# Performance work log

Hardware: AMD Instinct MI355X
Metric: run time of the kernel (lower is better)

## Reference

```python
import jax, jax.numpy as jnp
import numpy as np

WS = 8          # window size
SHIFT = WS // 2 # cyclic shift for shifted windows
HEADS = 6
C = 192
EMB = 256
HID = 4 * C
EPS = 1e-5


def _inorm(x):
    # InstanceNorm2d (affine=False): normalize each (sample, channel) over spatial dims
    m = x.mean(axis=(2, 3), keepdims=True)
    v = x.var(axis=(2, 3), keepdims=True)
    return (x - m) * jax.lax.rsqrt(v + EPS)


def _rel_index(ws):
    c = jnp.stack(jnp.meshgrid(jnp.arange(ws), jnp.arange(ws), indexing='ij'), -1).reshape(-1, 2)
    r = c[:, None] - c[None, :] + (ws - 1)          # (N,N,2) in [0, 2ws-2]
    return r[..., 0] * (2 * ws - 1) + r[..., 1]     # (N,N)


def _attn_mask(H, W, ws, shift):
    # standard Swin shifted-window mask: tokens from different pre-shift regions can't attend
    def ids(L):
        a = jnp.arange(L)
        return (a >= L - ws).astype(jnp.int32) + (a >= L - shift).astype(jnp.int32)
    img = ids(H)[:, None] * 3 + ids(W)[None, :]                     # (H,W)
    imgw = img.reshape(H // ws, ws, W // ws, ws).transpose(0, 2, 1, 3).reshape(-1, ws * ws)  # (nW,N)
    return jnp.where(imgw[:, None, :] != imgw[:, :, None], -1e9, 0.0)  # (nW,N,N)


def setup_inputs() -> dict:
    key = jax.random.key(0)
    ks = jax.random.split(key, 12)
    s = 0.02
    return {
        'x':        jax.random.normal(ks[0], (8, C, 128, 128), jnp.float32),
        'cond':     jax.random.normal(ks[1], (8, EMB), jnp.float32),
        'qkv_w':    jax.random.normal(ks[2], (3 * C, C), jnp.float32) * s,
        'qkv_b':    jnp.zeros((3 * C,), jnp.float32),
        'proj_w':   jax.random.normal(ks[3], (C, C), jnp.float32) * s,
        'proj_b':   jnp.zeros((C,), jnp.float32),
        'rel_bias': jax.random.normal(ks[4], ((2 * WS - 1) ** 2, HEADS), jnp.float32) * s,
        'film_w':   jax.random.normal(ks[5], (2 * C, EMB), jnp.float32) * s,
        'film_b':   jnp.zeros((2 * C,), jnp.float32),
        'mlp_w1':   jax.random.normal(ks[6], (HID, C), jnp.float32) * s,
        'mlp_b1':   jnp.zeros((HID,), jnp.float32),
        'mlp_w2':   jax.random.normal(ks[7], (C, HID), jnp.float32) * s,
        'mlp_b2':   jnp.zeros((C,), jnp.float32),
    }


def reference(x, cond, qkv_w, qkv_b, proj_w, proj_b, rel_bias,
              film_w, film_b, mlp_w1, mlp_b1, mlp_w2, mlp_b2):
    B, Cc, H, W = x.shape
    N = WS * WS
    nW = (H // WS) * (W // WS)
    hd = Cc // HEADS

    # ---- x = x + attn(norm1(x)) : shifted window attention ----
    xn = _inorm(x)
    xs = jnp.roll(xn, (-SHIFT, -SHIFT), axis=(2, 3))
    # window partition -> (B, nW, N, C)
    xw = (xs.reshape(B, Cc, H // WS, WS, W // WS, WS)
            .transpose(0, 2, 4, 3, 5, 1)
            .reshape(B, nW, N, Cc))
    qkv = xw @ qkv_w.T + qkv_b                       # (B,nW,N,3C)
    q, k, v = jnp.split(qkv, 3, axis=-1)
    def heads(t):
        return t.reshape(B, nW, N, HEADS, hd).transpose(0, 1, 3, 2, 4)  # (B,nW,H,N,hd)
    q, k, v = heads(q), heads(k), heads(v)
    attn = jnp.einsum('bwhnd,bwhmd->bwhnm', q, k) * (hd ** -0.5)
    bias = rel_bias[_rel_index(WS)].transpose(2, 0, 1)   # (HEADS,N,N)
    mask = _attn_mask(H, W, WS, SHIFT)                   # (nW,N,N)
    attn = attn + bias[None, None] + mask[None, :, None]
    a = jax.nn.softmax(attn, axis=-1)
    o = jnp.einsum('bwhnm,bwhmd->bwhnd', a, v)
    o = o.transpose(0, 1, 3, 2, 4).reshape(B, nW, N, Cc)
    o = o @ proj_w.T + proj_b
    # window reverse -> (B,C,H,W), undo shift
    o = (o.reshape(B, H // WS, W // WS, WS, WS, Cc)
           .transpose(0, 5, 1, 3, 2, 4)
           .reshape(B, Cc, H, W))
    o = jnp.roll(o, (SHIFT, SHIFT), axis=(2, 3))
    x = x + o

    # ---- x = x + mlp(FiLM(norm2(x), cond)) ----
    h = _inorm(x)
    gb = cond @ film_w.T + film_b                     # (B,2C)
    scale, shift = gb[:, :Cc], gb[:, Cc:]
    h = h * (1.0 + scale)[:, :, None, None] + shift[:, :, None, None]
    h = jnp.einsum('bchw,oc->bohw', h, mlp_w1) + mlp_b1[None, :, None, None]
    h = jax.nn.gelu(h, approximate=True)              # GELU('tanh')
    h = jnp.einsum('bchw,oc->bohw', h, mlp_w2) + mlp_b2[None, :, None, None]
    return x + h
```

## Files before the change

kernel.cpp:

```cpp
#include <hip/hip_runtime.h>
#include <hip/hip_bf16.h>

using bf16 = __hip_bfloat16;

#define HEADS 6
#define EPSV 1e-5f
#define QS 0.17677669529663687f

typedef __bf16 bfv8 __attribute__((ext_vector_type(8)));
typedef short sv8 __attribute__((ext_vector_type(8)));
typedef float fv4 __attribute__((ext_vector_type(4)));

__device__ __forceinline__ unsigned short f2bfbits(float f) {
  union { float f; unsigned u; } x{f};
  unsigned r = x.u + 0x7fffu + ((x.u >> 16) & 1u);
  return (unsigned short)(r >> 16);
}

__device__ __forceinline__ int swz(int row, int col, int rowstride) {
  return row * rowstride + ((((col >> 3) ^ (row & 7)) << 3) | (col & 7));
}

__device__ __forceinline__ uint2 pack4b(fv4 a, float b0, float b1, float b2, float b3) {
  uint2 r;
  r.x = (unsigned)f2bfbits(a[0] + b0) | ((unsigned)f2bfbits(a[1] + b1) << 16);
  r.y = (unsigned)f2bfbits(a[2] + b2) | ((unsigned)f2bfbits(a[3] + b3) << 16);
  return r;
}

template <bool BW>
__device__ __forceinline__ bfv8 ldwf(const short* wb, const float* wf, int row,
                                     int k, int ld, float scale) {
  if constexpr (BW) {
    return *(const bfv8*)(wb + (size_t)row * ld + k);
  } else {
    const float* p = wf + (size_t)row * ld + k;
    float4 a = *(const float4*)p;
    float4 b = *(const float4*)(p + 4);
    sv8 s;
    s[0] = (short)f2bfbits(a.x * scale); s[1] = (short)f2bfbits(a.y * scale);
    s[2] = (short)f2bfbits(a.z * scale); s[3] = (short)f2bfbits(a.w * scale);
    s[4] = (short)f2bfbits(b.x * scale); s[5] = (short)f2bfbits(b.y * scale);
    s[6] = (short)f2bfbits(b.z * scale); s[7] = (short)f2bfbits(b.w * scale);
    return __builtin_bit_cast(bfv8, s);
  }
}

__device__ __forceinline__ void stats_body(const float* __restrict__ x, int bc,
                                           float2* __restrict__ mr, int tid) {
  const float4* p = (const float4*)(x + (size_t)bc * 16384);
  float s = 0.f, s2 = 0.f;
  for (int i = tid; i < 4096; i += 256) {
    float4 v = p[i];
    s += v.x + v.y + v.z + v.w;
    s2 = fmaf(v.x, v.x, s2);
    s2 = fmaf(v.y, v.y, s2);
    s2 = fmaf(v.z, v.z, s2);
    s2 = fmaf(v.w, v.w, s2);
  }
#pragma unroll
  for (int off = 32; off > 0; off >>= 1) {
    s += __shfl_down(s, off);
    s2 += __shfl_down(s2, off);
  }
  __shared__ float rs[4], rs2[4];
  int wid = tid >> 6;
  if ((tid & 63) == 0) { rs[wid] = s; rs2[wid] = s2; }
  __syncthreads();
  if (tid == 0) {
    float S = rs[0] + rs[1] + rs[2] + rs[3];
    float S2 = rs2[0] + rs2[1] + rs2[2] + rs2[3];
    float m = S * (1.f / 16384.f);
    float v = S2 * (1.f / 16384.f) - m * m;
    mr[bc] = make_float2(m, rsqrtf(v + EPSV));
  }
}

__global__ __launch_bounds__(256) void stats_kernel(const float* __restrict__ x,
                                                    float2* __restrict__ mr) {
  stats_body(x, blockIdx.x, mr, threadIdx.x);
}

__device__ __forceinline__ void pack8(float4 a, float4 b, float sc, short* dst) {
  uint4 o;
  o.x = (unsigned)f2bfbits(a.x * sc) | ((unsigned)f2bfbits(a.y * sc) << 16);
  o.y = (unsigned)f2bfbits(a.z * sc) | ((unsigned)f2bfbits(a.w * sc) << 16);
  o.z = (unsigned)f2bfbits(b.x * sc) | ((unsigned)f2bfbits(b.y * sc) << 16);
  o.w = (unsigned)f2bfbits(b.z * sc) | ((unsigned)f2bfbits(b.w * sc) << 16);
  *(uint4*)dst = o;
}

__global__ __launch_bounds__(256) void fused_pre_kernel(
    const float* __restrict__ x, float2* __restrict__ mr1,
    const float* __restrict__ cond, const float* __restrict__ fw,
    const float* __restrict__ fb, float* __restrict__ gb,
    const float* __restrict__ qkv_w, const float* __restrict__ proj_w,
    const float* __restrict__ mlp_w1, const float* __restrict__ mlp_w2,
    short* __restrict__ wbA, int nUnits) {
  int bid = blockIdx.x;
  if (bid < 1536) {
    stats_body(x, bid, mr1, threadIdx.x);
    return;
  }
  bid -= 1536;
  if (bid < 12) {
    int g = bid * 256 + threadIdx.x;
    if (g >= 8 * 384) return;
    int b = g / 384, o = g % 384;
    const float* c = cond + b * 256;
    const float* w = fw + o * 256;
    float acc = fb[o];
    for (int k = 0; k < 256; k += 4) {
      float4 cv = *(const float4*)(c + k);
      float4 wv = *(const float4*)(w + k);
      acc = fmaf(cv.x, wv.x, acc);
      acc = fmaf(cv.y, wv.y, acc);
      acc = fmaf(cv.z, wv.z, acc);
      acc = fmaf(cv.w, wv.w, acc);
    }
    gb[g] = acc;
    return;
  }
  int u = (bid - 12) * 256 + threadIdx.x;
  if (u >= nUnits) return;
  if (u < 18432) {
    int e = u * 8;
    float sc = (e < 36864) ? QS : 1.f;
    const float* src = (e < 110592) ? (qkv_w + e) : (proj_w + (e - 110592));
    pack8(*(const float4*)src, *(const float4*)(src + 4), sc, wbA + e);
  } else if (u < 36864) {
    int f = (u - 18432) * 8;
    int ob = f / 12288, s = f % 12288;
    int row = s / 192, within = s % 192;
    int col0 = (((within >> 3) ^ (row & 7)) << 3);
    const float* src = mlp_w1 + (size_t)(ob * 64 + row) * 192 + col0;
    pack8(*(const float4*)src, *(const float4*)(src + 4), 1.f, wbA + 147456 + f);
  } else {
    int f = (u - 36864) * 8;
    int ob = f / 12288, s = f % 12288;
    int row = s / 64, within = s % 64;
    int ol = (((within >> 3) ^ (row & 7)) << 3);
    const float* src = mlp_w2 + (size_t)row * 768 + ob * 64 + ol;
    pack8(*(const float4*)src, *(const float4*)(src + 4), 1.f, wbA + 294912 + f);
  }
}

__global__ __launch_bounds__(64) void reduce2_kernel(const float2* __restrict__ part,
                                                     float2* __restrict__ mr2) {
  int bc = blockIdx.x;
  int b = bc / 192, c = bc % 192;
  const float2* p = part + (size_t)(b * 256) * 192 + c;
  float s = 0.f, q = 0.f;
  for (int k = threadIdx.x; k < 256; k += 64) {
    float2 v = p[(size_t)k * 192];
    s += v.x;
    q += v.y;
  }
#pragma unroll
  for (int off = 32; off > 0; off >>= 1) {
    s += __shfl_down(s, off);
    q += __shfl_down(q, off);
  }
  if (threadIdx.x == 0) {
    float m = s * (1.f / 16384.f);
    float v = q * (1.f / 16384.f) - m * m;
    mr2[bc] = make_float2(m, rsqrtf(v + EPSV));
  }
}

template <bool BW>
__global__ __launch_bounds__(512, 2) void attn_mfma4_kernel(
    const float* __restrict__ x, const float2* __restrict__ mr1,
    const short* __restrict__ wb, const float* __restrict__ qkv_w,
    const float* __restrict__ qkv_b, const float* __restrict__ proj_w,
    const float* __restrict__ proj_b, const float* __restrict__ rel_bias,
    float* __restrict__ out, float2* __restrict__ part) {
  __shared__ __align__(16) short s_x[64 * 192];
  __shared__ __align__(16) short s_k[64 * 192];
  __shared__ __align__(16) short s_v[192 * 64];
  __shared__ float s_rel[1350];

  const short* wbq = wb;
  const short* wbp = wb + 110592;

  int tid = threadIdx.x;
  int blk = ((blockIdx.x & 7) << 8) + (blockIdx.x >> 3);
  int b = blk >> 8;
  int wdw = blk & 255;
  int wh = wdw >> 4, ww = wdw & 15;
  int lane = tid & 63;
  int w = tid >> 6;
  int nloc = lane & 15, lg = lane >> 4;

  for (int i = tid; i < 1350; i += 512) s_rel[i] = rel_bias[i];

  for (int u = tid; u < 3072; u += 512) {
    int jh = u & 1, ii = (u >> 1) & 7, c = u >> 4;
    int hg = (wh * 8 + ii + 4) & 127;
    int wc0 = (ww * 8 + jh * 4 + 4) & 127;
    float4 v = *(const float4*)&x[((size_t)(b * 192 + c) << 14) + (hg << 7) + wc0];
    float2 mrv = mr1[b * 192 + c];
    int n0 = ii * 8 + jh * 4;
    s_x[swz(n0 + 0, c, 192)] = (short)f2bfbits((v.x - mrv.x) * mrv.y);
    s_x[swz(n0 + 1, c, 192)] = (short)f2bfbits((v.y - mrv.x) * mrv.y);
    s_x[swz(n0 + 2, c, 192)] = (short)f2bfbits((v.z - mrv.x) * mrv.y);
    s_x[swz(n0 + 3, c, 192)] = (short)f2bfbits((v.w - mrv.x) * mrv.y);
  }
  __syncthreads();

  for (int half = 0; half < 2; half++) {
    int ptb = half * 2;
    bfv8 xf[2][6];
#pragma unroll
    for (int pp = 0; pp < 2; pp++)
#pragma unroll
      for (int ks = 0; ks < 6; ks++)
        xf[pp][ks] = *(const bfv8*)&s_x[swz((ptb + pp) * 16 + nloc, ks * 32 + lg * 8, 192)];
    __syncthreads();

    bfv8 wf[6];
    {
      int t0 = w;
      int baserow0 = (t0 < 24) ? t0 * 16 : 384 + (t0 - 24) * 16;
      float scl0 = (!BW && t0 < 12) ? QS : 1.f;
#pragma unroll
      for (int ks = 0; ks < 6; ks++)
        wf[ks] = ldwf<BW>(wbq, qkv_w, baserow0 + nloc, ks * 32 + lg * 8, 192, scl0);
    }
    for (int t = w; t < 36;) {
      int tn = t + 8;
      bfv8 wfn[6];
      if (tn < 36) {
        int baserown = (tn < 24) ? tn * 16 : 384 + (tn - 24) * 16;
        float scln = (!BW && tn < 12) ? QS : 1.f;
#pragma unroll
        for (int ks = 0; ks < 6; ks++)
          wfn[ks] = ldwf<BW>(wbq, qkv_w, baserown + nloc, ks * 32 + lg * 8, 192, scln);
      }
      bool isQK = (t < 24);
#pragma unroll
      for (int pp = 0; pp < 2; pp++) {
        int pt = ptb + pp;
        fv4 acc = fv4{0.f, 0.f, 0.f, 0.f};
        if (isQK) {
#pragma unroll
          for (int ks = 0; ks < 6; ks++)
            acc = __builtin_amdgcn_mfma_f32_16x16x32_bf16(wf[ks], xf[pp][ks], acc, 0, 0, 0);
          int o0 = t * 16 + lg * 4;
          float4 bb = *(const float4*)&qkv_b[o0];
          float bsc = (t < 12) ? QS : 1.f;
          uint2 pkk = pack4b(acc, bb.x * bsc, bb.y * bsc, bb.z * bsc, bb.w * bsc);
          if (t < 12)
            *(uint2*)&s_x[swz(pt * 16 + nloc, o0, 192)] = pkk;
          else
            *(uint2*)&s_k[swz(pt * 16 + nloc, o0 - 192, 192)] = pkk;
        } else {
#pragma unroll
          for (int ks = 0; ks < 6; ks++)
            acc = __builtin_amdgcn_mfma_f32_16x16x32_bf16(xf[pp][ks], wf[ks], acc, 0, 0, 0);
          int d = (t - 24) * 16 + nloc;
          float bv = qkv_b[384 + d];
          *(uint2*)&s_v[swz(d, pt * 16 + lg * 4, 64)] = pack4b(acc, bv, bv, bv, bv);
        }
      }
      if (tn >= 36) break;
#pragma unroll
      for (int ks = 0; ks < 6; ks++) wf[ks] = wfn[ks];
      t = tn;
    }
  }
  __syncthreads();

  int maskh = (wh == 15), maskw = (ww == 15);
#pragma unroll
  for (int ui = 0; ui < 3; ui++) {
    int u = w * 3 + ui;
    int hh = u >> 2, ng = u & 3;
    int n = ng * 16 + nloc;
    int i1 = n >> 3, j1 = n & 7;
    int gn = (maskh ? (i1 < 4 ? 1 : 2) : 0) * 3 + (maskw ? (j1 < 4 ? 1 : 2) : 0);

    bfv8 qf = *(const bfv8*)&s_x[swz(n, hh * 32 + lg * 8, 192)];
    fv4 sc[4];
#pragma unroll
    for (int mt = 0; mt < 4; mt++) {
      bfv8 kf = *(const bfv8*)&s_k[swz(mt * 16 + nloc, hh * 32 + lg * 8, 192)];
      sc[mt] = __builtin_amdgcn_mfma_f32_16x16x32_bf16(kf, qf, fv4{0.f, 0.f, 0.f, 0.f}, 0, 0, 0);
    }
    bfv8 vfh[2][2];
#pragma unroll
    for (int dt = 0; dt < 2; dt++)
#pragma unroll
      for (int ks = 0; ks < 2; ks++)
        vfh[dt][ks] = *(const bfv8*)&s_v[swz(hh * 32 + dt * 16 + nloc, ks * 32 + lg * 8, 64)];

    float vals[16];
#pragma unroll
    for (int mt = 0; mt < 4; mt++) {
#pragma unroll
      for (int r = 0; r < 4; r++) {
        int m = mt * 16 + lg * 4 + r;
        int i2 = m >> 3, j2 = m & 7;
        int gm = (maskh ? (i2 < 4 ? 1 : 2) : 0) * 3 + (maskw ? (j2 < 4 ? 1 : 2) : 0);
        float v = sc[mt][r] + s_rel[((i1 - i2 + 7) * 15 + (j1 - j2 + 7)) * 6 + hh];
        vals[mt * 4 + r] = (gn == gm) ? v : v - 1e9f;
      }
    }
    float mx = vals[0];
#pragma unroll
    for (int q = 1; q < 16; q++) mx = fmaxf(mx, vals[q]);
    mx = fmaxf(mx, __shfl_xor(mx, 16));
    mx = fmaxf(mx, __shfl_xor(mx, 32));
    float sum = 0.f;
#pragma unroll
    for (int q = 0; q < 16; q++) {
      vals[q] = __expf(vals[q] - mx);
      sum += vals[q];
    }
    sum += __shfl_xor(sum, 16);
    sum += __shfl_xor(sum, 32);
    float inv = 1.f / sum;

    unsigned pk[4][2];
#pragma unroll
    for (int mt = 0; mt < 4; mt++) {
      pk[mt][0] = (unsigned)f2bfbits(vals[mt * 4] * inv) |
                  ((unsigned)f2bfbits(vals[mt * 4 + 1] * inv) << 16);
      pk[mt][1] = (unsigned)f2bfbits(vals[mt * 4 + 2] * inv) |
                  ((unsigned)f2bfbits(vals[mt * 4 + 3] * inv) << 16);
    }
    int sel = lg >> 1;
    int S0 = nloc + ((lg & 1) << 5);
    int S1 = S0 + 16;
    bfv8 pf[2];
#pragma unroll
    for (int ks = 0; ks < 2; ks++) {
      unsigned a0 = (unsigned)__shfl((int)pk[2 * ks][0], S0);
      unsigned b0 = (unsigned)__shfl((int)pk[2 * ks + 1][0], S0);
      unsigned a1 = (unsigned)__shfl((int)pk[2 * ks][1], S0);
      unsigned b1 = (unsigned)__shfl((int)pk[2 * ks + 1][1], S0);
      unsigned a2 = (unsigned)__shfl((int)pk[2 * ks][0], S1);
      unsigned b2 = (unsigned)__shfl((int)pk[2 * ks + 1][0], S1);
      unsigned a3 = (unsigned)__shfl((int)pk[2 * ks][1], S1);
      unsigned b3 = (unsigned)__shfl((int)pk[2 * ks + 1][1], S1);
      uint4 uu;
      uu.x = sel ? b0 : a0;
      uu.y = sel ? b1 : a1;
      uu.z = sel ? b2 : a2;
      uu.w = sel ? b3 : a3;
      pf[ks] = __builtin_bit_cast(bfv8, uu);
    }
#pragma unroll
    for (int dt = 0; dt < 2; dt++) {
      fv4 oa = fv4{0.f, 0.f, 0.f, 0.f};
#pragma unroll
      for (int ks = 0; ks < 2; ks++)
        oa = __builtin_amdgcn_mfma_f32_16x16x32_bf16(vfh[dt][ks], pf[ks], oa, 0, 0, 0);
      int d0 = hh * 32 + dt * 16 + lg * 4;
      *(uint2*)&s_x[swz(n, d0, 192)] = pack4b(oa, 0.f, 0.f, 0.f, 0.f);
    }
  }
  __syncthreads();

  {
    int a2 = w >> 1, half = w & 1;
    int hgv[2], wcv[2];
#pragma unroll
    for (int ni = 0; ni < 2; ni++) {
      int n = (half * 2 + ni) * 16 + nloc;
      hgv[ni] = (wh * 8 + (n >> 3) + 4) & 127;
      wcv[ni] = (ww * 8 + (n & 7) + 4) & 127;
    }
    float* redS = (float*)s_rel;
    float* redQ = redS + 384;

#pragma unroll
    for (int ci = 0; ci < 3; ci++) {
      int ct = a2 * 3 + ci;
      bfv8 wfp[6];
#pragma unroll
      for (int ks = 0; ks < 6; ks++)
        wfp[ks] = ldwf<BW>(wbp, proj_w, ct * 16 + nloc, ks * 32 + lg * 8, 192, 1.f);
      float xres[2][4];
#pragma unroll
      for (int ni = 0; ni < 2; ni++)
#pragma unroll
        for (int r = 0; r < 4; r++) {
          int c = ct * 16 + lg * 4 + r;
          xres[ni][r] = x[((size_t)(b * 192 + c) << 14) + (hgv[ni] << 7) + wcv[ni]];
        }
      float4 pb4 = *(const float4*)&proj_b[ct * 16 + lg * 4];
      const float* pbp = &pb4.x;
      float ssum[4] = {0.f, 0.f, 0.f, 0.f};
      float ssq[4] = {0.f, 0.f, 0.f, 0.f};
#pragma unroll
      for (int ni = 0; ni < 2; ni++) {
        int nt = half * 2 + ni;
        fv4 acc = fv4{0.f, 0.f, 0.f, 0.f};
#pragma unroll
        for (int ks = 0; ks < 6; ks++) {
          bfv8 of = *(const bfv8*)&s_x[swz(nt * 16 + nloc, ks * 32 + lg * 8, 192)];
          acc = __builtin_amdgcn_mfma_f32_16x16x32_bf16(wfp[ks], of, acc, 0, 0, 0);
        }
#pragma unroll
        for (int r = 0; r < 4; r++) {
          int c = ct * 16 + lg * 4 + r;
          size_t gi = ((size_t)(b * 192 + c) << 14) + (hgv[ni] << 7) + wcv[ni];
          float v = xres[ni][r] + acc[r] + pbp[r];
          out[gi] = v;
          ssum[r] += v;
          ssq[r] = fmaf(v, v, ssq[r]);
        }
      }
      if (part) {
#pragma unroll
        for (int r = 0; r < 4; r++) {
          float s = ssum[r], q = ssq[r];
#pragma unroll
          for (int m = 1; m < 16; m <<= 1) {
            s += __shfl_xor(s, m);
            q += __shfl_xor(q, m);
          }
          if (nloc == 0) {
            int c = ct * 16 + lg * 4 + r;
            redS[c * 2 + half] = s;
            redQ[c * 2 + half] = q;
          }
        }
      }
    }

    if (part) {
      __syncthreads();
      if (tid < 192) {
        float s = redS[tid * 2] + redS[tid * 2 + 1];
        float q = redQ[tid * 2] + redQ[tid * 2 + 1];
        part[(size_t)blk * 192 + tid] = make_float2(s, q);
      }
    }
  }
}

__global__ __launch_bounds__(512, 2) void mlp_mfma3_kernel(
    float* __restrict__ xio, const float2* __restrict__ mr2,
    const float* __restrict__ gb, const short* __restrict__ w1s,
    const short* __restrict__ w2s, const float* __restrict__ b1,
    const float* __restrict__ b2) {
  __shared__ __align__(16) short s_pool[128 * 192];
  __shared__ __align__(16) short s_h[128 * 64];
  __shared__ float s_b1[768];
  __shared__ float s_mean[192], s_rstd[192], s_scale[192], s_shift[192], s_b2[192];

  int tid = threadIdx.x;
  int blk = blockIdx.x;
  int b = blk >> 7;
  int p0 = (blk & 127) << 7;
  int lane = tid & 63;
  int w = tid >> 6;

  for (int i = tid; i < 768; i += 512) s_b1[i] = b1[i];
  for (int i = tid; i < 192; i += 512) {
    float2 mrv = mr2[b * 192 + i];
    s_mean[i] = mrv.x;
    s_rstd[i] = mrv.y;
    s_scale[i] = 1.f + gb[b * 384 + i];
    s_shift[i] = gb[b * 384 + 192 + i];
    s_b2[i] = b2[i];
  }
  __syncthreads();

  for (int e = tid; e < 768; e += 512) {
    int pq = e & 31, cb = e >> 5;
    int p = pq * 4, c0 = cb * 8;
    float4 xv[8];
#pragma unroll
    for (int j = 0; j < 8; j++)
      xv[j] = *(const float4*)&xio[((size_t)(b * 192 + c0 + j) << 14) + p0 + p];
#pragma unroll
    for (int j = 0; j < 8; j++) {
      int c = c0 + j;
      float mn = s_mean[c], rs = s_rstd[c], scv = s_scale[c], sh = s_shift[c];
      xv[j].x = (xv[j].x - mn) * rs * scv + sh;
      xv[j].y = (xv[j].y - mn) * rs * scv + sh;
      xv[j].z = (xv[j].z - mn) * rs * scv + sh;
      xv[j].w = (xv[j].w - mn) * rs * scv + sh;
    }
#pragma unroll
    for (int pp = 0; pp < 4; pp++) {
      sv8 pk;
#pragma unroll
      for (int j = 0; j < 8; j++) pk[j] = (short)f2bfbits((&xv[j].x)[pp]);
      *(sv8*)&s_pool[swz(p + pp, c0, 192)] = pk;
    }
  }
  __syncthreads();

  int prow = w * 16 + (lane & 15);
  bfv8 afr[6];
#pragma unroll
  for (int ks = 0; ks < 6; ks++) {
    int c = ks * 32 + (lane >> 4) * 8;
    afr[ks] = *(const bfv8*)&s_pool[swz(prow, c, 192)];
  }

  short* s_w1 = s_pool;
  short* s_w2 = s_pool + 12288;
  char* poolBytes = (char*)s_pool;

  fv4 acc2[12];
#pragma unroll
  for (int i = 0; i < 12; i++) acc2[i] = fv4{0.f, 0.f, 0.f, 0.f};

  for (int ob = 0; ob < 12; ob++) {
    __syncthreads();
    const char* g1 = (const char*)(w1s + ob * 12288);
    const char* g2 = (const char*)(w2s + ob * 12288);
#pragma unroll
    for (int i = 0; i < 3; i++) {
      int ch = w * 3 + i;
      __builtin_amdgcn_global_load_lds(
          (const __attribute__((address_space(1))) void*)(g1 + ch * 1024 + lane * 16),
          (__attribute__((address_space(3))) void*)(poolBytes + ch * 1024), 16, 0, 0);
      __builtin_amdgcn_global_load_lds(
          (const __attribute__((address_space(1))) void*)(g2 + ch * 1024 + lane * 16),
          (__attribute__((address_space(3))) void*)(poolBytes + 24576 + ch * 1024), 16, 0, 0);
    }
    __syncthreads();

#pragma unroll
    for (int it = 0; it < 4; it++) {
      fv4 a1 = fv4{0.f, 0.f, 0.f, 0.f};
      int orow = it * 16 + (lane & 15);
#pragma unroll
      for (int ks = 0; ks < 6; ks++) {
        int c = ks * 32 + (lane >> 4) * 8;
        bfv8 wf = *(const bfv8*)&s_w1[swz(orow, c, 192)];
        a1 = __builtin_amdgcn_mfma_f32_16x16x32_bf16(wf, afr[ks], a1, 0, 0, 0);
      }
      int o0 = ob * 64 + it * 16 + (lane >> 4) * 4;
      unsigned short hb[4];
#pragma unroll
      for (int r = 0; r < 4; r++) {
        float v = a1[r] + s_b1[o0 + r];
        float g = v / (1.f + __expf(-1.5957691216f * fmaf(0.044715f * v * v, v, v)));
        hb[r] = f2bfbits(g);
      }
      uint2 pk;
      pk.x = (unsigned)hb[0] | ((unsigned)hb[1] << 16);
      pk.y = (unsigned)hb[2] | ((unsigned)hb[3] << 16);
      int ol = it * 16 + (lane >> 4) * 4;
      *(uint2*)&s_h[swz(prow, ol, 64)] = pk;
    }

#pragma unroll
    for (int ks2 = 0; ks2 < 2; ks2++) {
      int ol = ks2 * 32 + (lane >> 4) * 8;
      bfv8 hf = *(const bfv8*)&s_h[swz(prow, ol, 64)];
#pragma unroll
      for (int it2 = 0; it2 < 12; it2++) {
        int crow = it2 * 16 + (lane & 15);
        bfv8 w2f = *(const bfv8*)&s_w2[swz(crow, ol, 64)];
        acc2[it2] = __builtin_amdgcn_mfma_f32_16x16x32_bf16(w2f, hf, acc2[it2], 0, 0, 0);
      }
    }
  }

  int p = p0 + w * 16 + (lane & 15);
#pragma unroll
  for (int it2 = 0; it2 < 12; it2++) {
    int c0 = it2 * 16 + (lane >> 4) * 4;
#pragma unroll
    for (int r = 0; r < 4; r++) {
      int c = c0 + r;
      size_t gi = ((size_t)(b * 192 + c) << 14) + p;
      xio[gi] += acc2[it2][r] + s_b2[c];
    }
  }
}

__global__ __launch_bounds__(512, 2) void mlp_mfma_kernel(
    float* __restrict__ xio, const float2* __restrict__ mr2,
    const float* __restrict__ gb, const float* __restrict__ w1,
    const float* __restrict__ b1, const float* __restrict__ w2,
    const float* __restrict__ b2) {
  __shared__ __align__(16) short s_a[128 * 192];
  __shared__ __align__(16) short s_h[128 * 64];
  __shared__ __align__(16) short s_w1[64 * 192];
  __shared__ __align__(16) short s_w2[192 * 64];
  __shared__ float s_b1[768];
  __shared__ float s_mean[192], s_rstd[192], s_scale[192], s_shift[192], s_b2[192];

  int tid = threadIdx.x;
  int blk = blockIdx.x;
  int b = blk >> 7;
  int p0 = (blk & 127) << 7;
  int lane = tid & 63;
  int w = tid >> 6;

  for (int i = tid; i < 768; i += 512) s_b1[i] = b1[i];
  for (int i = tid; i < 192; i += 512) {
    float2 mrv = mr2[b * 192 + i];
    s_mean[i] = mrv.x;
    s_rstd[i] = mrv.y;
    s_scale[i] = 1.f + gb[b * 384 + i];
    s_shift[i] = gb[b * 384 + 192 + i];
    s_b2[i] = b2[i];
  }
  __syncthreads();

  for (int e = tid; e < 3072; e += 512) {
    int p = e & 127, cb = e >> 7;
    int c0 = cb * 8;
    sv8 pk;
#pragma unroll
    for (int j = 0; j < 8; j++) {
      int c = c0 + j;
      float xv = xio[((size_t)(b * 192 + c) << 14) + p0 + p];
      float hn = (xv - s_mean[c]) * s_rstd[c];
      pk[j] = (short)f2bfbits(hn * s_scale[c] + s_shift[c]);
    }
    *(sv8*)&s_a[swz(p, c0, 192)] = pk;
  }
  __syncthreads();

  int prow = w * 16 + (lane & 15);
  bfv8 afr[6];
#pragma unroll
  for (int ks = 0; ks < 6; ks++) {
    int c = ks * 32 + (lane >> 4) * 8;
    afr[ks] = *(const bfv8*)&s_a[swz(prow, c, 192)];
  }

  fv4 acc2[12];
#pragma unroll
  for (int i = 0; i < 12; i++) acc2[i] = fv4{0.f, 0.f, 0.f, 0.f};

  for (int ob = 0; ob < 12; ob++) {
    __syncthreads();
    for (int e = tid; e < 3072; e += 512) {
      int row = e / 48, ch4 = e % 48;
      float4 v = *(const float4*)&w1[(size_t)(ob * 64 + row) * 192 + ch4 * 4];
      uint2 pk;
      pk.x = (unsigned)f2bfbits(v.x) | ((unsigned)f2bfbits(v.y) << 16);
      pk.y = (unsigned)f2bfbits(v.z) | ((unsigned)f2bfbits(v.w) << 16);
      *(uint2*)&s_w1[swz(row, ch4 * 4, 192)] = pk;
    }
    for (int e = tid; e < 3072; e += 512) {
      int row = e >> 4, o4 = (e & 15) * 4;
      float4 v = *(const float4*)&w2[(size_t)row * 768 + ob * 64 + o4];
      uint2 pk;
      pk.x = (unsigned)f2bfbits(v.x) | ((unsigned)f2bfbits(v.y) << 16);
      pk.y = (unsigned)f2bfbits(v.z) | ((unsigned)f2bfbits(v.w) << 16);
      *(uint2*)&s_w2[swz(row, o4, 64)] = pk;
    }
    __syncthreads();

#pragma unroll
    for (int it = 0; it < 4; it++) {
      fv4 a1 = fv4{0.f, 0.f, 0.f, 0.f};
      int orow = it * 16 + (lane & 15);
#pragma unroll
      for (int ks = 0; ks < 6; ks++) {
        int c = ks * 32 + (lane >> 4) * 8;
        bfv8 wf = *(const bfv8*)&s_w1[swz(orow, c, 192)];
        a1 = __builtin_amdgcn_mfma_f32_16x16x32_bf16(wf, afr[ks], a1, 0, 0, 0);
      }
      int o0 = ob * 64 + it * 16 + (lane >> 4) * 4;
      unsigned short hb[4];
#pragma unroll
      for (int r = 0; r < 4; r++) {
        float v = a1[r] + s_b1[o0 + r];
        float g = v / (1.f + __expf(-1.5957691216f * fmaf(0.044715f * v * v, v, v)));
        hb[r] = f2bfbits(g);
      }
      uint2 pk;
      pk.x = (unsigned)hb[0] | ((unsigned)hb[1] << 16);
      pk.y = (unsigned)hb[2] | ((unsigned)hb[3] << 16);
      int ol = it * 16 + (lane >> 4) * 4;
      *(uint2*)&s_h[swz(prow, ol, 64)] = pk;
    }

#pragma unroll
    for (int ks2 = 0; ks2 < 2; ks2++) {
      int ol = ks2 * 32 + (lane >> 4) * 8;
      bfv8 hf = *(const bfv8*)&s_h[swz(prow, ol, 64)];
#pragma unroll
      for (int it2 = 0; it2 < 12; it2++) {
        int crow = it2 * 16 + (lane & 15);
        bfv8 w2f = *(const bfv8*)&s_w2[swz(crow, ol, 64)];
        acc2[it2] = __builtin_amdgcn_mfma_f32_16x16x32_bf16(w2f, hf, acc2[it2], 0, 0, 0);
      }
    }
  }

  int p = p0 + w * 16 + (lane & 15);
#pragma unroll
  for (int it2 = 0; it2 < 12; it2++) {
    int c0 = it2 * 16 + (lane >> 4) * 4;
#pragma unroll
    for (int r = 0; r < 4; r++) {
      int c = c0 + r;
      size_t gi = ((size_t)(b * 192 + c) << 14) + p;
      xio[gi] += acc2[it2][r] + s_b2[c];
    }
  }
}

extern "C" void kernel_launch(void* const* d_in, const int* in_sizes, int n_in,
                              void* d_out, int out_size, void* d_ws, size_t ws_size,
                              hipStream_t stream) {
  const float* x = (const float*)d_in[0];
  const float* cond = (const float*)d_in[1];
  const float* qkv_w = (const float*)d_in[2];
  const float* qkv_b = (const float*)d_in[3];
  const float* proj_w = (const float*)d_in[4];
  const float* proj_b = (const float*)d_in[5];
  const float* rel_bias = (const float*)d_in[6];
  const float* film_w = (const float*)d_in[7];
  const float* film_b = (const float*)d_in[8];
  const float* mlp_w1 = (const float*)d_in[9];
  const float* mlp_b1 = (const float*)d_in[10];
  const float* mlp_w2 = (const float*)d_in[11];
  const float* mlp_b2 = (const float*)d_in[12];

  float* out = (float*)d_out;
  char* wsb = (char*)d_ws;

  float2* mr1 = (float2*)wsb;
  float2* mr2 = (float2*)(wsb + 12288);
  float* gb = (float*)(wsb + 24576);
  const size_t base = 36864;
  const size_t partB = 2048ull * 192 * 8;
  const size_t wbB = 442368ull * 2;

  bool fuseP = ws_size >= base + partB + wbB;
  bool haveM = fuseP || ws_size >= base + wbB;
  bool haveA = ws_size >= base + 294912;

  float2* part = fuseP ? (float2*)(wsb + base) : nullptr;
  short* wbA = (short*)(wsb + base + (fuseP ? partB : 0));

  int nUnits = haveM ? 55296 : (haveA ? 18432 : 0);
  fused_pre_kernel<<<1536 + 12 + (nUnits + 255) / 256, 256, 0, stream>>>(
      x, mr1, cond, film_w, film_b, gb, qkv_w, proj_w, mlp_w1, mlp_w2, wbA, nUnits);

  if (haveA)
    attn_mfma4_kernel<true><<<2048, 512, 0, stream>>>(
        x, mr1, wbA, qkv_w, qkv_b, proj_w, proj_b, rel_bias, out, part);
  else
    attn_mfma4_kernel<false><<<2048, 512, 0, stream>>>(
        x, mr1, wbA, qkv_w, qkv_b, proj_w, proj_b, rel_bias, out, part);

  if (part)
    reduce2_kernel<<<1536, 64, 0, stream>>>(part, mr2);
  else
    stats_kernel<<<1536, 256, 0, stream>>>(out, mr2);

  if (haveM)
    mlp_mfma3_kernel<<<1024, 512, 0, stream>>>(out, mr2, gb, wbA + 147456,
                                               wbA + 294912, mlp_b1, mlp_b2);
  else
    mlp_mfma_kernel<<<1024, 512, 0, stream>>>(out, mr2, gb, mlp_w1, mlp_b1,
                                              mlp_w2, mlp_b2);
}
```

Measured before the change: 423.8 us.

## Double-buffer MLP weight staging, raise attention occupancy, drop fused stats partials

The MLP kernel now streams weights in 32-row halves through two LDS buffers, prefetching the next half with global_load_lds while the current one is computed. The mlp_w2 prepack layout is changed to match a 32-column swizzle. The attention kernel gets a launch bound of 4 blocks per CU: it drops the software prefetch of qkv weights, loads V fragments lazily and reads the residual inline, all to cut register pressure. It also adds s_setprio around the MFMA sections. The fused per-window InstanceNorm partial sums and reduce kernel are removed in favour of a separate stats pass over the output, which adds a full extra read of the activation tensor.

```diff
diff --git a/kernel.cpp b/kernel.cpp
--- a/kernel.cpp
+++ b/kernel.cpp
@@ -19,6 +19,10 @@
 
 __device__ __forceinline__ int swz(int row, int col, int rowstride) {
   return row * rowstride + ((((col >> 3) ^ (row & 7)) << 3) | (col & 7));
+}
+
+__device__ __forceinline__ int swz32(int row, int col) {
+  return row * 32 + ((((col >> 3) ^ ((row >> 1) & 3)) << 3) | (col & 7));
 }
 
 __device__ __forceinline__ uint2 pack4b(fv4 a, float b0, float b1, float b2, float b3) {
@@ -137,44 +141,23 @@
     pack8(*(const float4*)src, *(const float4*)(src + 4), 1.f, wbA + 147456 + f);
   } else {
     int f = (u - 36864) * 8;
-    int ob = f / 12288, s = f % 12288;
-    int row = s / 64, within = s % 64;
-    int ol = (((within >> 3) ^ (row & 7)) << 3);
-    const float* src = mlp_w2 + (size_t)row * 768 + ob * 64 + ol;
+    int chunk = f / 6144, s = f % 6144;
+    int r = s / 32, within = s % 32;
+    int blk = within >> 3;
+    int ob = chunk >> 1, ch = chunk & 1;
+    int srccol = ob * 64 + ch * 32 + ((blk ^ ((r >> 1) & 3)) << 3);
+    const float* src = mlp_w2 + (size_t)r * 768 + srccol;
     pack8(*(const float4*)src, *(const float4*)(src + 4), 1.f, wbA + 294912 + f);
   }
 }
 
-__global__ __launch_bounds__(64) void reduce2_kernel(const float2* __restrict__ part,
-                                                     float2* __restrict__ mr2) {
-  int bc = blockIdx.x;
-  int b = bc / 192, c = bc % 192;
-  const float2* p = part + (size_t)(b * 256) * 192 + c;
-  float s = 0.f, q = 0.f;
-  for (int k = threadIdx.x; k < 256; k += 64) {
-    float2 v = p[(size_t)k * 192];
-    s += v.x;
-    q += v.y;
-  }
-#pragma unroll
-  for (int off = 32; off > 0; off >>= 1) {
-    s += __shfl_down(s, off);
-    q += __shfl_down(q, off);
-  }
-  if (threadIdx.x == 0) {
-    float m = s * (1.f / 16384.f);
-    float v = q * (1.f / 16384.f) - m * m;
-    mr2[bc] = make_float2(m, rsqrtf(v + EPSV));
-  }
-}
-
 template <bool BW>
-__global__ __launch_bounds__(512, 2) void attn_mfma4_kernel(
+__global__ __launch_bounds__(512, 4) void attn_mfma5_kernel(
     const float* __restrict__ x, const float2* __restrict__ mr1,
     const short* __restrict__ wb, const float* __restrict__ qkv_w,
     const float* __restrict__ qkv_b, const float* __restrict__ proj_w,
     const float* __restrict__ proj_b, const float* __restrict__ rel_bias,
-    float* __restrict__ out, float2* __restrict__ part) {
+    float* __restrict__ out) {
   __shared__ __align__(16) short s_x[64 * 192];
   __shared__ __align__(16) short s_k[64 * 192];
   __shared__ __align__(16) short s_v[192 * 64];
@@ -218,26 +201,15 @@
         xf[pp][ks] = *(const bfv8*)&s_x[swz((ptb + pp) * 16 + nloc, ks * 32 + lg * 8, 192)];
     __syncthreads();
 
-    bfv8 wf[6];
-    {
-      int t0 = w;
-      int baserow0 = (t0 < 24) ? t0 * 16 : 384 + (t0 - 24) * 16;
-      float scl0 = (!BW && t0 < 12) ? QS : 1.f;
+    for (int t = w; t < 36; t += 8) {
+      bool isQK = (t < 24);
+      int baserow = isQK ? t * 16 : 384 + (t - 24) * 16;
+      float scl = (!BW && t < 12) ? QS : 1.f;
+      bfv8 wf[6];
 #pragma unroll
       for (int ks = 0; ks < 6; ks++)
-        wf[ks] = ldwf<BW>(wbq, qkv_w, baserow0 + nloc, ks * 32 + lg * 8, 192, scl0);
-    }
-    for (int t = w; t < 36;) {
-      int tn = t + 8;
-      bfv8 wfn[6];
-      if (tn < 36) {
-        int baserown = (tn < 24) ? tn * 16 : 384 + (tn - 24) * 16;
-        float scln = (!BW && tn < 12) ? QS : 1.f;
-#pragma unroll
-        for (int ks = 0; ks < 6; ks++)
-          wfn[ks] = ldwf<BW>(wbq, qkv_w, baserown + nloc, ks * 32 + lg * 8, 192, scln);
-      }
-      bool isQK = (t < 24);
+        wf[ks] = ldwf<BW>(wbq, qkv_w, baserow + nloc, ks * 32 + lg * 8, 192, scl);
+      __builtin_amdgcn_s_setprio(1);
 #pragma unroll
       for (int pp = 0; pp < 2; pp++) {
         int pt = ptb + pp;
@@ -263,10 +235,7 @@
           *(uint2*)&s_v[swz(d, pt * 16 + lg * 4, 64)] = pack4b(acc, bv, bv, bv, bv);
         }
       }
-      if (tn >= 36) break;
-#pragma unroll
-      for (int ks = 0; ks < 6; ks++) wf[ks] = wfn[ks];
-      t = tn;
+      __builtin_amdgcn_s_setprio(0);
     }
   }
   __syncthreads();
@@ -282,18 +251,13 @@
 
     bfv8 qf = *(const bfv8*)&s_x[swz(n, hh * 32 + lg * 8, 192)];
     fv4 sc[4];
+    __builtin_amdgcn_s_setprio(1);
 #pragma unroll
     for (int mt = 0; mt < 4; mt++) {
       bfv8 kf = *(const bfv8*)&s_k[swz(mt * 16 + nloc, hh * 32 + lg * 8, 192)];
       sc[mt] = __builtin_amdgcn_mfma_f32_16x16x32_bf16(kf, qf, fv4{0.f, 0.f, 0.f, 0.f}, 0, 0, 0);
     }
-    bfv8 vfh[2][2];
-#pragma unroll
-    for (int dt = 0; dt < 2; dt++)
-#pragma unroll
-      for (int ks = 0; ks < 2; ks++)
-        vfh[dt][ks] = *(const bfv8*)&s_v[swz(hh * 32 + dt * 16 + nloc, ks * 32 + lg * 8, 64)];
-
+    __builtin_amdgcn_s_setprio(0);
     float vals[16];
 #pragma unroll
     for (int mt = 0; mt < 4; mt++) {
@@ -350,104 +314,66 @@
       uu.w = sel ? b3 : a3;
       pf[ks] = __builtin_bit_cast(bfv8, uu);
     }
+    __builtin_amdgcn_s_setprio(1);
 #pragma unroll
     for (int dt = 0; dt < 2; dt++) {
       fv4 oa = fv4{0.f, 0.f, 0.f, 0.f};
 #pragma unroll
-      for (int ks = 0; ks < 2; ks++)
-        oa = __builtin_amdgcn_mfma_f32_16x16x32_bf16(vfh[dt][ks], pf[ks], oa, 0, 0, 0);
+      for (int ks = 0; ks < 2; ks++) {
+        bfv8 vf = *(const bfv8*)&s_v[swz(hh * 32 + dt * 16 + nloc, ks * 32 + lg * 8, 64)];
+        oa = __builtin_amdgcn_mfma_f32_16x16x32_bf16(vf, pf[ks], oa, 0, 0, 0);
+      }
       int d0 = hh * 32 + dt * 16 + lg * 4;
       *(uint2*)&s_x[swz(n, d0, 192)] = pack4b(oa, 0.f, 0.f, 0.f, 0.f);
     }
+    __builtin_amdgcn_s_setprio(0);
   }
   __syncthreads();
 
   {
     int a2 = w >> 1, half = w & 1;
-    int hgv[2], wcv[2];
-#pragma unroll
-    for (int ni = 0; ni < 2; ni++) {
-      int n = (half * 2 + ni) * 16 + nloc;
-      hgv[ni] = (wh * 8 + (n >> 3) + 4) & 127;
-      wcv[ni] = (ww * 8 + (n & 7) + 4) & 127;
-    }
-    float* redS = (float*)s_rel;
-    float* redQ = redS + 384;
-
 #pragma unroll
     for (int ci = 0; ci < 3; ci++) {
       int ct = a2 * 3 + ci;
-      bfv8 wfp[6];
+      bfv8 wf[6];
 #pragma unroll
       for (int ks = 0; ks < 6; ks++)
-        wfp[ks] = ldwf<BW>(wbp, proj_w, ct * 16 + nloc, ks * 32 + lg * 8, 192, 1.f);
-      float xres[2][4];
-#pragma unroll
-      for (int ni = 0; ni < 2; ni++)
-#pragma unroll
-        for (int r = 0; r < 4; r++) {
-          int c = ct * 16 + lg * 4 + r;
-          xres[ni][r] = x[((size_t)(b * 192 + c) << 14) + (hgv[ni] << 7) + wcv[ni]];
-        }
-      float4 pb4 = *(const float4*)&proj_b[ct * 16 + lg * 4];
-      const float* pbp = &pb4.x;
-      float ssum[4] = {0.f, 0.f, 0.f, 0.f};
-      float ssq[4] = {0.f, 0.f, 0.f, 0.f};
+        wf[ks] = ldwf<BW>(wbp, proj_w, ct * 16 + nloc, ks * 32 + lg * 8, 192, 1.f);
 #pragma unroll
       for (int ni = 0; ni < 2; ni++) {
         int nt = half * 2 + ni;
         fv4 acc = fv4{0.f, 0.f, 0.f, 0.f};
+        __builtin_amdgcn_s_setprio(1);
 #pragma unroll
         for (int ks = 0; ks < 6; ks++) {
           bfv8 of = *(const bfv8*)&s_x[swz(nt * 16 + nloc, ks * 32 + lg * 8, 192)];
-          acc = __builtin_amdgcn_mfma_f32_16x16x32_bf16(wfp[ks], of, acc, 0, 0, 0);
+          acc = __builtin_amdgcn_mfma_f32_16x16x32_bf16(wf[ks], of, acc, 0, 0, 0);
         }
+        __builtin_amdgcn_s_setprio(0);
+        int n = nt * 16 + nloc;
+        int ii = n >> 3, jj = n & 7;
+        int hg = (wh * 8 + ii + 4) & 127;
+        int wc = (ww * 8 + jj + 4) & 127;
+        float4 pb4 = *(const float4*)&proj_b[ct * 16 + lg * 4];
+        const float* pbp = &pb4.x;
 #pragma unroll
         for (int r = 0; r < 4; r++) {
           int c = ct * 16 + lg * 4 + r;
-          size_t gi = ((size_t)(b * 192 + c) << 14) + (hgv[ni] << 7) + wcv[ni];
-          float v = xres[ni][r] + acc[r] + pbp[r];
-          out[gi] = v;
-          ssum[r] += v;
-          ssq[r] = fmaf(v, v, ssq[r]);
+          size_t gi = ((size_t)(b * 192 + c) << 14) + (hg << 7) + wc;
+          out[gi] = x[gi] + acc[r] + pbp[r];
         }
       }
-      if (part) {
-#pragma unroll
-        for (int r = 0; r < 4; r++) {
-          float s = ssum[r], q = ssq[r];
-#pragma unroll
-          for (int m = 1; m < 16; m <<= 1) {
-            s += __shfl_xor(s, m);
-            q += __shfl_xor(q, m);
-          }
-          if (nloc == 0) {
-            int c = ct * 16 + lg * 4 + r;
-            redS[c * 2 + half] = s;
-            redQ[c * 2 + half] = q;
-          }
-        }
-      }
-    }
-
-    if (part) {
-      __syncthreads();
-      if (tid < 192) {
-        float s = redS[tid * 2] + redS[tid * 2 + 1];
-        float q = redQ[tid * 2] + redQ[tid * 2 + 1];
-        part[(size_t)blk * 192 + tid] = make_float2(s, q);
-      }
-    }
-  }
-}
-
-__global__ __launch_bounds__(512, 2) void mlp_mfma3_kernel(
+    }
+  }
+}
+
+__global__ __launch_bounds__(512, 2) void mlp_mfma5_kernel(
     float* __restrict__ xio, const float2* __restrict__ mr2,
     const float* __restrict__ gb, const short* __restrict__ w1s,
     const short* __restrict__ w2s, const float* __restrict__ b1,
     const float* __restrict__ b2) {
-  __shared__ __align__(16) short s_pool[128 * 192];
-  __shared__ __align__(16) short s_h[128 * 64];
+  __shared__ __align__(16) short s_pool[2 * 12288];
+  __shared__ __align__(16) short s_h[128 * 32];
   __shared__ float s_b1[768];
   __shared__ float s_mean[192], s_rstd[192], s_scale[192], s_shift[192], s_b2[192];
 
@@ -502,68 +428,83 @@
     int c = ks * 32 + (lane >> 4) * 8;
     afr[ks] = *(const bfv8*)&s_pool[swz(prow, c, 192)];
   }
-
-  short* s_w1 = s_pool;
-  short* s_w2 = s_pool + 12288;
+  __syncthreads();
+
   char* poolBytes = (char*)s_pool;
+  const char* w1B = (const char*)w1s;
+  const char* w2B = (const char*)w2s;
 
   fv4 acc2[12];
 #pragma unroll
   for (int i = 0; i < 12; i++) acc2[i] = fv4{0.f, 0.f, 0.f, 0.f};
 
-  for (int ob = 0; ob < 12; ob++) {
-    __syncthreads();
-    const char* g1 = (const char*)(w1s + ob * 12288);
-    const char* g2 = (const char*)(w2s + ob * 12288);
-#pragma unroll
-    for (int i = 0; i < 3; i++) {
-      int ch = w * 3 + i;
-      __builtin_amdgcn_global_load_lds(
-          (const __attribute__((address_space(1))) void*)(g1 + ch * 1024 + lane * 16),
-          (__attribute__((address_space(3))) void*)(poolBytes + ch * 1024), 16, 0, 0);
-      __builtin_amdgcn_global_load_lds(
-          (const __attribute__((address_space(1))) void*)(g2 + ch * 1024 + lane * 16),
-          (__attribute__((address_space(3))) void*)(poolBytes + 24576 + ch * 1024), 16, 0, 0);
-    }
-    __syncthreads();
-
-#pragma unroll
-    for (int it = 0; it < 4; it++) {
+#define STAGE_HALF(hb, bufIdx)                                                        \
+  {                                                                                   \
+    char* dstB = poolBytes + (bufIdx)*24576;                                          \
+    _Pragma("unroll") for (int j = 0; j < 3; j++) {                                   \
+      int ch = w * 3 + j;                                                             \
+      const char* srcB = (ch < 12) ? (w1B + (size_t)(hb)*12288 + ch * 1024)           \
+                                   : (w2B + (size_t)(hb)*12288 + (ch - 12) * 1024);   \
+      __builtin_amdgcn_global_load_lds(                                               \
+          (const __attribute__((address_space(1))) void*)(srcB + lane * 16),          \
+          (__attribute__((address_space(3))) void*)(dstB + ch * 1024), 16, 0, 0);     \
+    }                                                                                 \
+  }
+
+  STAGE_HALF(0, 0);
+  asm volatile("s_waitcnt vmcnt(0)" ::: "memory");
+  __builtin_amdgcn_s_barrier();
+
+  for (int i = 0; i < 24; ++i) {
+    int cur = i & 1;
+    if (i < 23) STAGE_HALF(i + 1, cur ^ 1);
+
+    const short* bw1 = s_pool + cur * 12288;
+    const short* bw2 = s_pool + cur * 12288 + 6144;
+
+#pragma unroll
+    for (int it = 0; it < 2; it++) {
       fv4 a1 = fv4{0.f, 0.f, 0.f, 0.f};
       int orow = it * 16 + (lane & 15);
+      __builtin_amdgcn_s_setprio(1);
 #pragma unroll
       for (int ks = 0; ks < 6; ks++) {
         int c = ks * 32 + (lane >> 4) * 8;
-        bfv8 wf = *(const bfv8*)&s_w1[swz(orow, c, 192)];
+        bfv8 wf = *(const bfv8*)&bw1[swz(orow, c, 192)];
         a1 = __builtin_amdgcn_mfma_f32_16x16x32_bf16(wf, afr[ks], a1, 0, 0, 0);
       }
-      int o0 = ob * 64 + it * 16 + (lane >> 4) * 4;
-      unsigned short hb[4];
+      __builtin_amdgcn_s_setprio(0);
+      int o0 = i * 32 + it * 16 + (lane >> 4) * 4;
+      unsigned short hbv[4];
 #pragma unroll
       for (int r = 0; r < 4; r++) {
         float v = a1[r] + s_b1[o0 + r];
         float g = v / (1.f + __expf(-1.5957691216f * fmaf(0.044715f * v * v, v, v)));
-        hb[r] = f2bfbits(g);
+        hbv[r] = f2bfbits(g);
       }
       uint2 pk;
-      pk.x = (unsigned)hb[0] | ((unsigned)hb[1] << 16);
-      pk.y = (unsigned)hb[2] | ((unsigned)hb[3] << 16);
+      pk.x = (unsigned)hbv[0] | ((unsigned)hbv[1] << 16);
+      pk.y = (unsigned)hbv[2] | ((unsigned)hbv[3] << 16);
       int ol = it * 16 + (lane >> 4) * 4;
-      *(uint2*)&s_h[swz(prow, ol, 64)] = pk;
-    }
-
-#pragma unroll
-    for (int ks2 = 0; ks2 < 2; ks2++) {
-      int ol = ks2 * 32 + (lane >> 4) * 8;
-      bfv8 hf = *(const bfv8*)&s_h[swz(prow, ol, 64)];
-#pragma unroll
-      for (int it2 = 0; it2 < 12; it2++) {
-        int crow = it2 * 16 + (lane & 15);
-        bfv8 w2f = *(const bfv8*)&s_w2[swz(crow, ol, 64)];
-        acc2[it2] = __builtin_amdgcn_mfma_f32_16x16x32_bf16(w2f, hf, acc2[it2], 0, 0, 0);
-      }
-    }
-  }
+      *(uint2*)&s_h[swz32(prow, ol)] = pk;
+    }
+
+    bfv8 hf = *(const bfv8*)&s_h[swz32(prow, (lane >> 4) * 8)];
+    __builtin_amdgcn_s_setprio(1);
+#pragma unroll
+    for (int it2 = 0; it2 < 12; it2++) {
+      int crow = it2 * 16 + (lane & 15);
+      bfv8 w2f = *(const bfv8*)&bw2[swz32(crow, (lane >> 4) * 8)];
+      acc2[it2] = __builtin_amdgcn_mfma_f32_16x16x32_bf16(w2f, hf, acc2[it2], 0, 0, 0);
+    }
+    __builtin_amdgcn_s_setprio(0);
+
+    if (i < 23) {
+      asm volatile("s_waitcnt vmcnt(0)" ::: "memory");
+      __builtin_amdgcn_s_barrier();
+    }
+  }
+#undef STAGE_HALF
 
   int p = p0 + w * 16 + (lane & 15);
 #pragma unroll
@@ -730,34 +671,27 @@
   float2* mr2 = (float2*)(wsb + 12288);
   float* gb = (float*)(wsb + 24576);
   const size_t base = 36864;
-  const size_t partB = 2048ull * 192 * 8;
   const size_t wbB = 442368ull * 2;
-
-  bool fuseP = ws_size >= base + partB + wbB;
-  bool haveM = fuseP || ws_size >= base + wbB;
+  short* wbA = (short*)(wsb + base);
+
   bool haveA = ws_size >= base + 294912;
-
-  float2* part = fuseP ? (float2*)(wsb + base) : nullptr;
-  short* wbA = (short*)(wsb + base + (fuseP ? partB : 0));
+  bool haveM = ws_size >= base + wbB;
 
   int nUnits = haveM ? 55296 : (haveA ? 18432 : 0);
   fused_pre_kernel<<<1536 + 12 + (nUnits + 255) / 256, 256, 0, stream>>>(
       x, mr1, cond, film_w, film_b, gb, qkv_w, proj_w, mlp_w1, mlp_w2, wbA, nUnits);
 
   if (haveA)
-    attn_mfma4_kernel<true><<<2048, 512, 0, stream>>>(
-        x, mr1, wbA, qkv_w, qkv_b, proj_w, proj_b, rel_bias, out, part);
+    attn_mfma5_kernel<true><<<2048, 512, 0, stream>>>(
+        x, mr1, wbA, qkv_w, qkv_b, proj_w, proj_b, rel_bias, out);
   else
-    attn_mfma4_kernel<false><<<2048, 512, 0, stream>>>(
-        x, mr1, wbA, qkv_w, qkv_b, proj_w, proj_b, rel_bias, out, part);
-
-  if (part)
-    reduce2_kernel<<<1536, 64, 0, stream>>>(part, mr2);
-  else
-    stats_kernel<<<1536, 256, 0, stream>>>(out, mr2);
+    attn_mfma5_kernel<false><<<2048, 512, 0, stream>>>(
+        x, mr1, wbA, qkv_w, qkv_b, proj_w, proj_b, rel_bias, out);
+
+  stats_kernel<<<1536, 256, 0, stream>>>(out, mr2);
 
   if (haveM)
-    mlp_mfma3_kernel<<<1024, 512, 0, stream>>>(out, mr2, gb, wbA + 147456,
+    mlp_mfma5_kernel<<<1024, 512, 0, stream>>>(out, mr2, gb, wbA + 147456,
                                                wbA + 294912, mlp_b1, mlp_b2);
   else
     mlp_mfma_kernel<<<1024, 512, 0, stream>>>(out, mr2, gb, mlp_w1, mlp_b1,
```

Measured after the change: 382.0 us, median of 2. 1.11x faster.
